# Optimization experiments

Hardware: AMD Instinct MI355X
Metric: run time of the kernel (lower is better)

Reference implementation:

```python
import jax, jax.numpy as jnp
import numpy as np

N_ADDR, N_TX = 150000, 200000
IN_DIM, HID, HEADS = 64, 32, 4
DIM = HID // HEADS
E_AT, E_TA, E_AA = 1000000, 1000000, 500000
SLOPE = 0.2  # HANConv default negative_slope


def setup_inputs() -> dict:
    key = jax.random.key(0)
    ks = jax.random.split(key, 16)
    f = lambda k, shape, s: jax.random.normal(k, shape, dtype=jnp.float32) * s
    return {
        "x_addr": f(ks[0], (N_ADDR, IN_DIM), 1.0),
        "x_tx": f(ks[1], (N_TX, IN_DIM), 1.0),
        "e_at_src": jax.random.randint(ks[2], (E_AT,), 0, N_ADDR, dtype=jnp.int32),
        "e_at_dst": jax.random.randint(ks[3], (E_AT,), 0, N_TX, dtype=jnp.int32),
        "e_ta_src": jax.random.randint(ks[4], (E_TA,), 0, N_TX, dtype=jnp.int32),
        "e_ta_dst": jax.random.randint(ks[5], (E_TA,), 0, N_ADDR, dtype=jnp.int32),
        "e_aa_src": jax.random.randint(ks[6], (E_AA,), 0, N_ADDR, dtype=jnp.int32),
        "e_aa_dst": jax.random.randint(ks[7], (E_AA,), 0, N_ADDR, dtype=jnp.int32),
        "pW1": f(ks[8], (2, IN_DIM, HID), 0.1),      # layer-1 proj per node type [addr, tx]
        "pb1": jnp.zeros((2, HID), jnp.float32),
        "pW23": f(ks[9], (2, 2, HID, HID), 0.1),     # [layer-1, node_type]
        "pb23": jnp.zeros((2, 2, HID), jnp.float32),
        "att_src": f(ks[10], (3, 3, HEADS, DIM), 0.1),  # [layer, edge_type, H, D]
        "att_dst": f(ks[11], (3, 3, HEADS, DIM), 0.1),
        "kW": f(ks[12], (3, HID, HID), 0.1),         # semantic k_lin per layer
        "kb": jnp.zeros((3, HID), jnp.float32),
        "q": f(ks[13], (3, HID), 0.1),               # semantic query per layer
        "linW": f(ks[14], (HID, 2), 0.1),
        "linb": jnp.zeros((2,), jnp.float32),
    }


def _edge_softmax(logits, dst, n):
    # numerically stable segment softmax over destination neighborhoods
    m = jax.ops.segment_max(logits, dst, num_segments=n)          # [n, H]
    m = jnp.where(jnp.isfinite(m), m, 0.0)
    e = jnp.exp(logits - m[dst])
    s = jax.ops.segment_sum(e, dst, num_segments=n)
    return e / (s[dst] + 1e-16)


def _relation(h_src, h_dst, src, dst, a_s, a_d, n_dst):
    alpha_src = jnp.einsum('nhd,hd->nh', h_src, a_s)
    alpha_dst = jnp.einsum('nhd,hd->nh', h_dst, a_d)
    logit = alpha_src[src] + alpha_dst[dst]                        # [E, H]
    logit = jnp.where(logit >= 0, logit, SLOPE * logit)            # leaky_relu
    alpha = _edge_softmax(logit, dst, n_dst)
    msg = h_src[src] * alpha[:, :, None]                           # [E, H, D]
    out = jax.ops.segment_sum(msg, dst, num_segments=n_dst)        # [n_dst, H, D]
    return jax.nn.relu(out.reshape(n_dst, HID))


def _semantic(xs, kW, kb, q):
    # xs: [R, N, F]; semantic-level attention over R relations (PyG `group`)
    t = jnp.tanh(xs @ kW + kb).mean(axis=1)       # [R, F]
    attn = jax.nn.softmax((t * q).sum(-1))        # [R]
    return jnp.einsum('r,rnf->nf', attn, xs)


def _han_layer(x_a, x_t, Wa, ba, Wt, bt, a_s, a_d, kW, kb, q, edges):
    h_a = (x_a @ Wa + ba).reshape(-1, HEADS, DIM)
    h_t = (x_t @ Wt + bt).reshape(-1, HEADS, DIM)
    o_tx = _relation(h_a, h_t, edges[0], edges[1], a_s[0], a_d[0], N_TX)
    o_a1 = _relation(h_t, h_a, edges[2], edges[3], a_s[1], a_d[1], N_ADDR)
    o_a2 = _relation(h_a, h_a, edges[4], edges[5], a_s[2], a_d[2], N_ADDR)
    new_a = _semantic(jnp.stack([o_a1, o_a2]), kW, kb, q)
    new_t = _semantic(o_tx[None], kW, kb, q)
    return new_a, new_t


def reference(x_addr, x_tx, e_at_src, e_at_dst, e_ta_src, e_ta_dst,
              e_aa_src, e_aa_dst, pW1, pb1, pW23, pb23, att_src, att_dst,
              kW, kb, q, linW, linb):
    edges = (e_at_src, e_at_dst, e_ta_src, e_ta_dst, e_aa_src, e_aa_dst)
    a, t = _han_layer(x_addr, x_tx, pW1[0], pb1[0], pW1[1], pb1[1],
                      att_src[0], att_dst[0], kW[0], kb[0], q[0], edges)
    a, t = jax.nn.relu(a), jax.nn.relu(t)  # wrapper relu; dropout = eval identity
    for l in range(2):
        a, t = _han_layer(a, t, pW23[l, 0], pb23[l, 0], pW23[l, 1], pb23[l, 1],
                          att_src[l + 1], att_dst[l + 1],
                          kW[l + 1], kb[l + 1], q[l + 1], edges)
        a, t = jax.nn.relu(a), jax.nn.relu(t)
    return a @ linW + linb
```

## Files before the change

### kernel.cpp

```cpp
#include <hip/hip_runtime.h>
#include <hip/hip_bf16.h>
#include <hip/hip_fp16.h>

#define NA 150000
#define NT 200000
#define E_AT 1000000
#define E_TA 1000000
#define E_AA 500000

#define CHK 4096
#define CAP 8192
#define P_AT 391
#define P_TA 293
#define P_AA 293
#define NBINS (P_AT + P_TA + P_AA)
#define CB_AT 245
#define CB_TA 245
#define CB_AA 123
#define NBBIN (CB_AT + CB_TA + CB_AA)

#define GB_AT 6250
#define GB_TA 4688
#define GB_AA 4688

#define GA32 4688
#define GT32 6250
#define NB_SEM 586

#define WO_W1   0
#define WO_B1   4096
#define WO_W23  4160
#define WO_B23  8256
#define WO_AS   8384
#define WO_AD   8672
#define WO_KW   8960
#define WO_KB   12032
#define WO_Q    12128
#define WO_LW   12224
#define WO_LB   12288

__device__ __forceinline__ float ldf(const void* p, long i, int f32) {
    if (f32) return ((const float*)p)[i];
    unsigned int u = ((const unsigned short*)p)[i];
    union { unsigned int ui; float f; } v; v.ui = u << 16;
    return v.f;
}
__device__ __forceinline__ float bf2f(unsigned short u) {
    union { unsigned int ui; float f; } v; v.ui = ((unsigned int)u) << 16;
    return v.f;
}
__device__ __forceinline__ float h2f(unsigned short u) {
    return __half2float(__ushort_as_half(u));
}
__device__ __forceinline__ unsigned short f2h(float x) {
    return __half_as_ushort(__float2half(x));
}
__device__ __forceinline__ float ftanh(float x) {
    x = fminf(fmaxf(x, -9.f), 9.f);
    float e = __expf(2.f * x);
    return (e - 1.f) / (e + 1.f);
}

__global__ void k_init(const void* __restrict__ x,
                       const void* __restrict__ pW1, const void* __restrict__ pb1,
                       const void* __restrict__ pW23, const void* __restrict__ pb23,
                       const void* __restrict__ attS, const void* __restrict__ attD,
                       const void* __restrict__ kW, const void* __restrict__ kb,
                       const void* __restrict__ qv, const void* __restrict__ linW,
                       const void* __restrict__ linb,
                       float* __restrict__ wts, int* __restrict__ flagp,
                       int* __restrict__ gcnt, float* __restrict__ sem) {
    __shared__ int cnt;
    const int t = threadIdx.x;
    if (t == 0) cnt = 0;
    __syncthreads();
    const unsigned short* u = (const unsigned short*)x;
    int wild = 0;
    for (int i = t; i < 4096; i += 256) {
        unsigned short v = u[i];
        int e = (v >> 7) & 0xFF;
        if (e > 133 || (e != 0 && e < 100)) wild++;
        else if (e == 0 && (v & 0x7F)) wild++;
    }
    atomicAdd(&cnt, wild);
    __syncthreads();
    const int f32 = (cnt > 1024) ? 1 : 0;
    if (t == 0) *flagp = f32;
    if (t < 8) sem[t] = 0.f;
    for (int i = t; i < 1024; i += 256) gcnt[i] = 0;
    for (int i = t; i < 4096; i += 256) wts[WO_W1 + i]  = ldf(pW1, i, f32);
    for (int i = t; i < 64;   i += 256) wts[WO_B1 + i]  = ldf(pb1, i, f32);
    for (int i = t; i < 4096; i += 256) wts[WO_W23 + i] = ldf(pW23, i, f32);
    for (int i = t; i < 128;  i += 256) wts[WO_B23 + i] = ldf(pb23, i, f32);
    for (int i = t; i < 288;  i += 256) wts[WO_AS + i]  = ldf(attS, i, f32);
    for (int i = t; i < 288;  i += 256) wts[WO_AD + i]  = ldf(attD, i, f32);
    for (int i = t; i < 3072; i += 256) wts[WO_KW + i]  = ldf(kW, i, f32);
    for (int i = t; i < 96;   i += 256) wts[WO_KB + i]  = ldf(kb, i, f32);
    for (int i = t; i < 96;   i += 256) wts[WO_Q + i]   = ldf(qv, i, f32);
    for (int i = t; i < 64;   i += 256) wts[WO_LW + i]  = ldf(linW, i, f32);
    for (int i = t; i < 2;    i += 256) wts[WO_LB + i]  = ldf(linb, i, f32);
}

__global__ __launch_bounds__(256) void k_projbin(
        const void* __restrict__ Xa, const void* __restrict__ Xt,
        const float* __restrict__ W, const float* __restrict__ Bv,
        unsigned short* __restrict__ Ha, unsigned short* __restrict__ Ht,
        const float* __restrict__ attD,
        float* __restrict__ ad0, float* __restrict__ ad1, float* __restrict__ ad2,
        const int* __restrict__ flagp,
        const int* __restrict__ eat_s, const int* __restrict__ eat_d,
        const int* __restrict__ eta_s, const int* __restrict__ eta_d,
        const int* __restrict__ eaa_s, const int* __restrict__ eaa_d,
        int* __restrict__ gcnt,
        int* __restrict__ slot_at, int* __restrict__ slot_ta, int* __restrict__ slot_aa) {
    __shared__ float smem[4224];
    const int t = threadIdx.x;
    int b = blockIdx.x;
    if (b < NBBIN) {
        int* hist = (int*)smem;
        const int *src, *dst; int E, P, seg; int* slot;
        if (b < CB_AT)              { src = eat_s; dst = eat_d; E = E_AT; P = P_AT; seg = 0;            slot = slot_at; }
        else if (b < CB_AT + CB_TA) { b -= CB_AT;  src = eta_s; dst = eta_d; E = E_TA; P = P_TA; seg = P_AT;        slot = slot_ta; }
        else                        { b -= CB_AT + CB_TA; src = eaa_s; dst = eaa_d; E = E_AA; P = P_AA; seg = P_AT + P_TA; slot = slot_aa; }
        long e0 = (long)b * CHK;
        for (int i = t; i < P; i += 256) hist[i] = 0;
        __syncthreads();
        for (int k = 0; k < CHK; k += 256) {
            long e = e0 + k + t;
            if (e < E) atomicAdd(&hist[dst[e] >> 9], 1);
        }
        __syncthreads();
        for (int i = t; i < P; i += 256) {
            int v = hist[i];
            hist[i] = atomicAdd(&gcnt[seg + i], v);
        }
        __syncthreads();
        for (int k = 0; k < CHK; k += 256) {
            long e = e0 + k + t;
            if (e < E) {
                int d = dst[e];
                int bin = d >> 9;
                int pos = atomicAdd(&hist[bin], 1);
                slot[bin * CAP + pos] = ((d & 511) << 18) | src[e];
            }
        }
        return;
    }
    b -= NBBIN;
    constexpr int K = 64, XS = K + 4, CPR = K / 4, TOT4 = 32 * CPR;
    float* Xs = smem;
    float* Wl = smem + 2176;
    const bool isA = b < GA32;
    const int bb = isA ? b : b - GA32;
    const int N = isA ? NA : NT;
    const int wOff = isA ? 0 : 2048;
    const int bOff = isA ? 0 : 32;
    const long n0 = (long)bb * 32;
    for (int i = t; i < K * 32; i += 256) Wl[i] = W[wOff + i];
    {
        const void* X = isA ? Xa : Xt;
        const int f32 = *flagp;
        if (f32) {
            const float* Xf = (const float*)X;
            for (int i = t; i < TOT4; i += 256) {
                int r = i / CPR, c = (i - r * CPR) * 4;
                long gr = n0 + r; if (gr >= N) gr = N - 1;
                *(float4*)&Xs[r * XS + c] = *(const float4*)&Xf[gr * K + c];
            }
        } else {
            const unsigned short* Xh = (const unsigned short*)X;
            for (int i = t; i < TOT4; i += 256) {
                int r = i / CPR, c = (i - r * CPR) * 4;
                long gr = n0 + r; if (gr >= N) gr = N - 1;
                ushort4 v = *(const ushort4*)&Xh[gr * K + c];
                float4 o;
                o.x = bf2f(v.x); o.y = bf2f(v.y); o.z = bf2f(v.z); o.w = bf2f(v.w);
                *(float4*)&Xs[r * XS + c] = o;
            }
        }
    }
    __syncthreads();
    const int g = t >> 3, q = t & 7;
    const long n = n0 + g;
    float a0 = Bv[bOff + q * 4 + 0];
    float a1 = Bv[bOff + q * 4 + 1];
    float a2 = Bv[bOff + q * 4 + 2];
    float a3 = Bv[bOff + q * 4 + 3];
#pragma unroll 4
    for (int k4 = 0; k4 < K; k4 += 4) {
        float4 xv = *(const float4*)&Xs[g * XS + k4];
        float4 w0 = *(const float4*)&Wl[(k4 + 0) * 32 + q * 4];
        float4 w1 = *(const float4*)&Wl[(k4 + 1) * 32 + q * 4];
        float4 w2 = *(const float4*)&Wl[(k4 + 2) * 32 + q * 4];
        float4 w3 = *(const float4*)&Wl[(k4 + 3) * 32 + q * 4];
        a0 = fmaf(xv.x, w0.x, a0); a1 = fmaf(xv.x, w0.y, a1);
        a2 = fmaf(xv.x, w0.z, a2); a3 = fmaf(xv.x, w0.w, a3);
        a0 = fmaf(xv.y, w1.x, a0); a1 = fmaf(xv.y, w1.y, a1);
        a2 = fmaf(xv.y, w1.z, a2); a3 = fmaf(xv.y, w1.w, a3);
        a0 = fmaf(xv.z, w2.x, a0); a1 = fmaf(xv.z, w2.y, a1);
        a2 = fmaf(xv.z, w2.z, a2); a3 = fmaf(xv.z, w2.w, a3);
        a0 = fmaf(xv.w, w3.x, a0); a1 = fmaf(xv.w, w3.y, a1);
        a2 = fmaf(xv.w, w3.z, a2); a3 = fmaf(xv.w, w3.w, a3);
    }
    if (n < N) {
        unsigned short* Hh = isA ? Ha : Ht;
        unsigned int p01 = (unsigned)f2h(a0) | ((unsigned)f2h(a1) << 16);
        unsigned int p23 = (unsigned)f2h(a2) | ((unsigned)f2h(a3) << 16);
        *(uint2*)&Hh[n * 32 + q * 4] = make_uint2(p01, p23);
        const int hh = q >> 1;
        const int ai = q * 4;
        if (isA) {
            float p1 = a0 * attD[ai + 32] + a1 * attD[ai + 33]
                     + a2 * attD[ai + 34] + a3 * attD[ai + 35];
            float p2 = a0 * attD[ai + 64] + a1 * attD[ai + 65]
                     + a2 * attD[ai + 66] + a3 * attD[ai + 67];
            float s1 = p1 + __shfl_xor(p1, 1);
            float s2 = p2 + __shfl_xor(p2, 1);
            if (!(q & 1)) { ad1[n * 4 + hh] = s1; ad2[n * 4 + hh] = s2; }
        } else {
            float p0 = a0 * attD[ai] + a1 * attD[ai + 1]
                     + a2 * attD[ai + 2] + a3 * attD[ai + 3];
            float s0 = p0 + __shfl_xor(p0, 1);
            if (!(q & 1)) ad0[n * 4 + hh] = s0;
        }
    }
}

__global__ __launch_bounds__(256) void k_proj2(
        const float* __restrict__ O1, const float* __restrict__ Ot,
        const float* __restrict__ O2, const float* __restrict__ semL,
        const float* __restrict__ W, int wOffA, int wOffT,
        const float* __restrict__ Bv, int bOffA, int bOffT,
        unsigned short* __restrict__ Ha, unsigned short* __restrict__ Ht,
        const float* __restrict__ attD, int lBase,
        float* __restrict__ ad0, float* __restrict__ ad1, float* __restrict__ ad2) {
    constexpr int K = 32, XS = K + 4, CPR = K / 4, TOT4 = 32 * CPR;
    __shared__ float Xs[32 * XS];
    __shared__ float Wl[K * 32];
    const int t = threadIdx.x;
    const bool isA = blockIdx.x < GA32;
    const int bb = isA ? (int)blockIdx.x : (int)blockIdx.x - GA32;
    const int N = isA ? NA : NT;
    const int wOff = isA ? wOffA : wOffT;
    const int bOff = isA ? bOffA : bOffT;
    const long n0 = (long)bb * 32;
    for (int i = t; i < K * 32; i += 256) Wl[i] = W[wOff + i];
    if (isA) {
        float s0 = semL[0] * (1.0f / NA), s1 = semL[1] * (1.0f / NA);
        float m = fmaxf(s0, s1);
        float e0 = __expf(s0 - m), e1 = __expf(s1 - m);
        float inv = 1.f / (e0 + e1);
        const float w0 = e0 * inv, w1 = e1 * inv;
        for (int i = t; i < TOT4; i += 256) {
            int r = i / CPR, c = (i - r * CPR) * 4;
            long gr = n0 + r; if (gr >= N) gr = N - 1;
            float4 va = *(const float4*)&O1[gr * K + c];
            float4 vb = *(const float4*)&O2[gr * K + c];
            float4 o;
            o.x = fmaxf(w0 * va.x + w1 * vb.x, 0.f);
            o.y = fmaxf(w0 * va.y + w1 * vb.y, 0.f);
            o.z = fmaxf(w0 * va.z + w1 * vb.z, 0.f);
            o.w = fmaxf(w0 * va.w + w1 * vb.w, 0.f);
            *(float4*)&Xs[r * XS + c] = o;
        }
    } else {
        for (int i = t; i < TOT4; i += 256) {
            int r = i / CPR, c = (i - r * CPR) * 4;
            long gr = n0 + r; if (gr >= N) gr = N - 1;
            *(float4*)&Xs[r * XS + c] = *(const float4*)&Ot[gr * K + c];
        }
    }
    __syncthreads();
    const int g = t >> 3, q = t & 7;
    const long n = n0 + g;
    float a0 = Bv[bOff + q * 4 + 0];
    float a1 = Bv[bOff + q * 4 + 1];
    float a2 = Bv[bOff + q * 4 + 2];
    float a3 = Bv[bOff + q * 4 + 3];
#pragma unroll 4
    for (int k4 = 0; k4 < K; k4 += 4) {
        float4 xv = *(const float4*)&Xs[g * XS + k4];
        float4 w0 = *(const float4*)&Wl[(k4 + 0) * 32 + q * 4];
        float4 w1 = *(const float4*)&Wl[(k4 + 1) * 32 + q * 4];
        float4 w2 = *(const float4*)&Wl[(k4 + 2) * 32 + q * 4];
        float4 w3 = *(const float4*)&Wl[(k4 + 3) * 32 + q * 4];
        a0 = fmaf(xv.x, w0.x, a0); a1 = fmaf(xv.x, w0.y, a1);
        a2 = fmaf(xv.x, w0.z, a2); a3 = fmaf(xv.x, w0.w, a3);
        a0 = fmaf(xv.y, w1.x, a0); a1 = fmaf(xv.y, w1.y, a1);
        a2 = fmaf(xv.y, w1.z, a2); a3 = fmaf(xv.y, w1.w, a3);
        a0 = fmaf(xv.z, w2.x, a0); a1 = fmaf(xv.z, w2.y, a1);
        a2 = fmaf(xv.z, w2.z, a2); a3 = fmaf(xv.z, w2.w, a3);
        a0 = fmaf(xv.w, w3.x, a0); a1 = fmaf(xv.w, w3.y, a1);
        a2 = fmaf(xv.w, w3.z, a2); a3 = fmaf(xv.w, w3.w, a3);
    }
    if (n < N) {
        unsigned short* Hh = isA ? Ha : Ht;
        unsigned int p01 = (unsigned)f2h(a0) | ((unsigned)f2h(a1) << 16);
        unsigned int p23 = (unsigned)f2h(a2) | ((unsigned)f2h(a3) << 16);
        *(uint2*)&Hh[n * 32 + q * 4] = make_uint2(p01, p23);
        const int hh = q >> 1;
        const int ai = lBase + q * 4;
        if (isA) {
            float p1 = a0 * attD[ai + 32] + a1 * attD[ai + 33]
                     + a2 * attD[ai + 34] + a3 * attD[ai + 35];
            float p2 = a0 * attD[ai + 64] + a1 * attD[ai + 65]
                     + a2 * attD[ai + 66] + a3 * attD[ai + 67];
            float s1 = p1 + __shfl_xor(p1, 1);
            float s2 = p2 + __shfl_xor(p2, 1);
            if (!(q & 1)) { ad1[n * 4 + hh] = s1; ad2[n * 4 + hh] = s2; }
        } else {
            float p0 = a0 * attD[ai] + a1 * attD[ai + 1]
                     + a2 * attD[ai + 2] + a3 * attD[ai + 3];
            float s0 = p0 + __shfl_xor(p0, 1);
            if (!(q & 1)) ad0[n * 4 + hh] = s0;
        }
    }
}

__global__ void k_binscan(const int* __restrict__ gcnt, int* __restrict__ bbase,
                          int* __restrict__ off_at, int* __restrict__ off_ta,
                          int* __restrict__ off_aa) {
    __shared__ int sa[512], sb[512];
    int t = threadIdx.x;
    const int segs[4] = {0, P_AT, P_AT + P_TA, NBINS};
    for (int r = 0; r < 3; r++) {
        int s0 = segs[r], P = segs[r + 1] - s0;
        sa[t] = (t < P) ? gcnt[s0 + t] : 0;
        __syncthreads();
        int* in = sa; int* out = sb;
        for (int o = 1; o < 512; o <<= 1) {
            out[t] = in[t] + (t >= o ? in[t - o] : 0);
            __syncthreads();
            int* tmp = in; in = out; out = tmp;
        }
        if (t < P) bbase[s0 + t] = (t ? in[t - 1] : 0);
        __syncthreads();
    }
    if (t == 0) { off_at[NT] = E_AT; off_ta[NA] = E_TA; off_aa[NA] = E_AA; }
}

__global__ __launch_bounds__(256) void k_binsort(
        const int* __restrict__ gcnt, const int* __restrict__ bbase,
        const int* __restrict__ slot_at, const int* __restrict__ slot_ta,
        const int* __restrict__ slot_aa,
        int* __restrict__ off_at, int* __restrict__ off_ta, int* __restrict__ off_aa,
        int* __restrict__ csr_at, int* __restrict__ csr_ta, int* __restrict__ csr_aa) {
    __shared__ int sa[512], sb[512], cur[512];
    int b = blockIdx.x, t = threadIdx.x;
    const int* slot; int* off; int* csr; int N, bin, seg;
    if (b < P_AT)              { slot = slot_at; off = off_at; csr = csr_at; N = NT; bin = b;                seg = 0; }
    else if (b < P_AT + P_TA)  { slot = slot_ta; off = off_ta; csr = csr_ta; N = NA; bin = b - P_AT;         seg = P_AT; }
    else                       { slot = slot_aa; off = off_aa; csr = csr_aa; N = NA; bin = b - P_AT - P_TA;  seg = P_AT + P_TA; }
    const int cnt  = gcnt[seg + bin];
    const int base = bbase[seg + bin];
    const int* sp = &slot[bin * CAP];
    sa[t] = 0; sa[t + 256] = 0;
    __syncthreads();
    for (int i = t; i < cnt; i += 256) atomicAdd(&sa[sp[i] >> 18], 1);
    __syncthreads();
    int* in = sa; int* out = sb;
    for (int o = 1; o < 512; o <<= 1) {
        for (int i = t; i < 512; i += 256)
            out[i] = in[i] + (i >= o ? in[i - o] : 0);
        __syncthreads();
        int* tmp = in; in = out; out = tmp;
    }
    for (int i = t; i < 512; i += 256) {
        int excl = i ? in[i - 1] : 0;
        cur[i] = excl;
        int gd = bin * 512 + i;
        if (gd < N) off[gd] = base + excl;
    }
    __syncthreads();
    for (int i = t; i < cnt; i += 256) {
        int pk = sp[i];
        int pos = atomicAdd(&cur[pk >> 18], 1);
        csr[base + pos] = pk & 0x3FFFF;
    }
}

__global__ __launch_bounds__(256) void k_gather3(
        const int* __restrict__ off_at, const int* __restrict__ csr_at,
        const int* __restrict__ off_ta, const int* __restrict__ csr_ta,
        const int* __restrict__ off_aa, const int* __restrict__ csr_aa,
        const float* __restrict__ ad0, const float* __restrict__ ad1,
        const float* __restrict__ ad2,
        const unsigned short* __restrict__ h_a, const unsigned short* __restrict__ h_t,
        float* __restrict__ o_tx, float* __restrict__ o_a1, float* __restrict__ o_a2,
        const float* __restrict__ attS, int lBase) {
    int b = blockIdx.x;
    const int *off, *csr;
    const float *ad_;
    const unsigned short* Hs;
    float* O;
    int N, attOff;
    if (b < GB_AT) {
        off = off_at; csr = csr_at; ad_ = ad0; Hs = h_a; O = o_tx; N = NT;
        attOff = lBase;
    } else if (b < GB_AT + GB_TA) {
        b -= GB_AT;
        off = off_ta; csr = csr_ta; ad_ = ad1; Hs = h_t; O = o_a1; N = NA;
        attOff = lBase + 32;
    } else {
        b -= GB_AT + GB_TA;
        off = off_aa; csr = csr_aa; ad_ = ad2; Hs = h_a; O = o_a2; N = NA;
        attOff = lBase + 64;
    }
    const int t = threadIdx.x;
    const int q = t & 7;
    const int hh = q >> 1;
    const int n = b * 32 + (t >> 3);
    if (n >= N) return;
    const float4 aq = *(const float4*)&attS[attOff + q * 4];
    const float aq0 = aq.x, aq1 = aq.y, aq2 = aq.z, aq3 = aq.w;
    const float adv = ad_[n * 4 + hh];
    const int p0 = off[n], p1 = off[n + 1];
    float ax = 0.f, ay = 0.f, az = 0.f, aw = 0.f, se = 0.f;
    int p = p0;
    for (; p + 4 <= p1; p += 4) {
        int s0 = csr[p], s1 = csr[p + 1], s2 = csr[p + 2], s3 = csr[p + 3];
        ushort4 v0 = *(const ushort4*)&Hs[s0 * 32 + q * 4];
        ushort4 v1 = *(const ushort4*)&Hs[s1 * 32 + q * 4];
        ushort4 v2 = *(const ushort4*)&Hs[s2 * 32 + q * 4];
        ushort4 v3 = *(const ushort4*)&Hs[s3 * 32 + q * 4];
        float h00 = h2f(v0.x), h01 = h2f(v0.y), h02 = h2f(v0.z), h03 = h2f(v0.w);
        float h10 = h2f(v1.x), h11 = h2f(v1.y), h12 = h2f(v1.z), h13 = h2f(v1.w);
        float h20 = h2f(v2.x), h21 = h2f(v2.y), h22 = h2f(v2.z), h23 = h2f(v2.w);
        float h30 = h2f(v3.x), h31 = h2f(v3.y), h32 = h2f(v3.z), h33 = h2f(v3.w);
        float pt0 = h00 * aq0 + h01 * aq1 + h02 * aq2 + h03 * aq3;
        float pt1 = h10 * aq0 + h11 * aq1 + h12 * aq2 + h13 * aq3;
        float pt2 = h20 * aq0 + h21 * aq1 + h22 * aq2 + h23 * aq3;
        float pt3 = h30 * aq0 + h31 * aq1 + h32 * aq2 + h33 * aq3;
        float al0 = pt0 + __shfl_xor(pt0, 1);
        float al1 = pt1 + __shfl_xor(pt1, 1);
        float al2 = pt2 + __shfl_xor(pt2, 1);
        float al3 = pt3 + __shfl_xor(pt3, 1);
        float l0 = al0 + adv; l0 = fmaxf(l0, 0.2f * l0); float e0 = __expf(l0);
        float l1 = al1 + adv; l1 = fmaxf(l1, 0.2f * l1); float e1 = __expf(l1);
        float l2 = al2 + adv; l2 = fmaxf(l2, 0.2f * l2); float e2 = __expf(l2);
        float l3 = al3 + adv; l3 = fmaxf(l3, 0.2f * l3); float e3 = __expf(l3);
        se += e0 + e1 + e2 + e3;
        ax += e0 * h00 + e1 * h10 + e2 * h20 + e3 * h30;
        ay += e0 * h01 + e1 * h11 + e2 * h21 + e3 * h31;
        az += e0 * h02 + e1 * h12 + e2 * h22 + e3 * h32;
        aw += e0 * h03 + e1 * h13 + e2 * h23 + e3 * h33;
    }
    for (; p < p1; p++) {
        int s = csr[p];
        ushort4 v = *(const ushort4*)&Hs[s * 32 + q * 4];
        float h0 = h2f(v.x), h1 = h2f(v.y), h2 = h2f(v.z), h3 = h2f(v.w);
        float pt = h0 * aq0 + h1 * aq1 + h2 * aq2 + h3 * aq3;
        float al = pt + __shfl_xor(pt, 1);
        float l = al + adv; l = fmaxf(l, 0.2f * l);
        float e = __expf(l);
        se += e;
        ax += e * h0; ay += e * h1; az += e * h2; aw += e * h3;
    }
    const float inv = 1.f / (se + 1e-16f);
    float4 r;
    r.x = fmaxf(ax * inv, 0.f);
    r.y = fmaxf(ay * inv, 0.f);
    r.z = fmaxf(az * inv, 0.f);
    r.w = fmaxf(aw * inv, 0.f);
    *(float4*)&O[n * 32 + q * 4] = r;
}

__global__ __launch_bounds__(256) void k_sem_reduce(
        const float* __restrict__ O1, const float* __restrict__ O2,
        const float* __restrict__ kWl, const float* __restrict__ kbl,
        const float* __restrict__ qvl, float* __restrict__ semL) {
    __shared__ float w[1088];
    __shared__ float bacc;
    const int t = threadIdx.x;
    const int r = (blockIdx.x >= NB_SEM) ? 1 : 0;
    const float* O = r ? O2 : O1;
    for (int i = t; i < 1024; i += 256) w[i] = kWl[i];
    if (t < 32) w[1024 + t] = kbl[t];
    if (t >= 64 && t < 96) w[1056 + (t - 64)] = qvl[t - 64];
    if (t == 0) bacc = 0.f;
    __syncthreads();
    long n = (long)(blockIdx.x - r * NB_SEM) * 256 + t;
    float S = 0.f;
    if (n < NA) {
        float x[32];
#pragma unroll
        for (int k = 0; k < 32; k++) x[k] = O[n * 32 + k];
#pragma unroll
        for (int f = 0; f < 32; f++) {
            float acc = w[1024 + f];
#pragma unroll
            for (int k = 0; k < 32; k++) acc += x[k] * w[k * 32 + f];
            S += ftanh(acc) * w[1056 + f];
        }
    }
    for (int o = 32; o > 0; o >>= 1) S += __shfl_xor(S, o, 64);
    if ((t & 63) == 0) atomicAdd(&bacc, S);
    __syncthreads();
    if (t == 0) atomicAdd(&semL[r], bacc);
}

__global__ void k_combine_final(const float* __restrict__ o1, const float* __restrict__ o2,
                                const float* __restrict__ semL,
                                const float* __restrict__ linW, const float* __restrict__ linb,
                                void* __restrict__ out, int N, const int* __restrict__ flagp) {
    int n = blockIdx.x * blockDim.x + threadIdx.x;
    if (n >= N) return;
    int f32 = *flagp;
    float q0 = semL[0] * (1.0f / NA), q1 = semL[1] * (1.0f / NA);
    float m = fmaxf(q0, q1);
    float e0 = __expf(q0 - m), e1 = __expf(q1 - m);
    float ai = 1.f / (e0 + e1);
    float w0 = e0 * ai, w1 = e1 * ai;
    float s0 = linb[0], s1 = linb[1];
    const float* p1 = &o1[(long)n * 32];
    const float* p2 = &o2[(long)n * 32];
#pragma unroll
    for (int f = 0; f < 32; f++) {
        float v = w0 * p1[f] + w1 * p2[f];
        v = (v > 0.f) ? v : 0.f;
        s0 += v * linW[f * 2];
        s1 += v * linW[f * 2 + 1];
    }
    if (f32) { ((float*)out)[n * 2] = s0; ((float*)out)[n * 2 + 1] = s1; }
    else {
        ((__hip_bfloat16*)out)[n * 2] = __float2bfloat16(s0);
        ((__hip_bfloat16*)out)[n * 2 + 1] = __float2bfloat16(s1);
    }
}

static inline int gblocks(long n) { return (int)((n + 255) / 256); }

extern "C" void kernel_launch(void* const* d_in, const int* in_sizes, int n_in,
                              void* d_out, int out_size, void* d_ws, size_t ws_size,
                              hipStream_t stream) {
    const void* x_addr = d_in[0];
    const void* x_tx   = d_in[1];
    const int* eat_s = (const int*)d_in[2];
    const int* eat_d = (const int*)d_in[3];
    const int* eta_s = (const int*)d_in[4];
    const int* eta_d = (const int*)d_in[5];
    const int* eaa_s = (const int*)d_in[6];
    const int* eaa_d = (const int*)d_in[7];
    const void* pW1  = d_in[8];
    const void* pb1  = d_in[9];
    const void* pW23 = d_in[10];
    const void* pb23 = d_in[11];
    const void* attS = d_in[12];
    const void* attD = d_in[13];
    const void* kW   = d_in[14];
    const void* kb   = d_in[15];
    const void* qv   = d_in[16];
    const void* linW = d_in[17];
    const void* linb = d_in[18];

    const size_t NA32 = (size_t)NA * 32, NT32 = (size_t)NT * 32;
    const size_t NA4 = (size_t)NA * 4, NT4 = (size_t)NT * 4;

    float* ws    = (float*)d_ws;
    float* h_aF  = ws;
    float* h_tF  = h_aF + NA32;
    float* o_a1  = h_tF + NT32;
    float* o_a2  = o_a1 + NA32;
    float* o_tx  = o_a2 + NA32;
    float* ad1   = o_tx + NT32;
    float* ad2   = ad1 + NA4;
    float* ad0   = ad2 + NA4;
    float* sem   = ad0 + NT4;
    int*   flagp = (int*)(sem + 8);
    int*   off_at = flagp + 16;
    int*   off_ta = off_at + (NT + 1);
    int*   off_aa = off_ta + (NA + 1);
    int*   csr_at = off_aa + (NA + 1);
    int*   csr_ta = csr_at + E_AT;
    int*   csr_aa = csr_ta + E_TA;
    int*   gcnt   = csr_aa + E_AA;
    int*   bbase  = gcnt + 1024;
    int*   slot_at = bbase + 1024;
    int*   slot_ta = slot_at + P_AT * CAP;
    int*   slot_aa = slot_ta + P_TA * CAP;
    float* wts    = (float*)(slot_aa + (size_t)P_AA * CAP);

    unsigned short* h_a = (unsigned short*)h_aF;
    unsigned short* h_t = (unsigned short*)h_tF;

    k_init<<<1, 256, 0, stream>>>(x_addr, pW1, pb1, pW23, pb23, attS, attD,
                                  kW, kb, qv, linW, linb, wts, flagp, gcnt, sem);

    k_projbin<<<NBBIN + GA32 + GT32, 256, 0, stream>>>(
        x_addr, x_tx, wts + WO_W1, wts + WO_B1, h_a, h_t, wts + WO_AD,
        ad0, ad1, ad2, flagp,
        eat_s, eat_d, eta_s, eta_d, eaa_s, eaa_d,
        gcnt, slot_at, slot_ta, slot_aa);
    k_binscan<<<1, 512, 0, stream>>>(gcnt, bbase, off_at, off_ta, off_aa);
    k_binsort<<<NBINS, 256, 0, stream>>>(gcnt, bbase, slot_at, slot_ta, slot_aa,
                                         off_at, off_ta, off_aa, csr_at, csr_ta, csr_aa);

    for (int l = 0; l < 3; l++) {
        if (l > 0) {
            int wi = (l - 1) * 2;
            k_proj2<<<GA32 + GT32, 256, 0, stream>>>(
                o_a1, o_tx, o_a2, sem + 2 * (l - 1),
                wts + WO_W23, (wi + 0) * 1024, (wi + 1) * 1024,
                wts + WO_B23, (wi + 0) * 32, (wi + 1) * 32,
                h_a, h_t, wts + WO_AD, l * 96, ad0, ad1, ad2);
        }
        k_gather3<<<GB_AT + GB_TA + GB_AA, 256, 0, stream>>>(
            off_at, csr_at, off_ta, csr_ta, off_aa, csr_aa,
            ad0, ad1, ad2, h_a, h_t, o_tx, o_a1, o_a2, wts + WO_AS, l * 96);
        k_sem_reduce<<<2 * NB_SEM, 256, 0, stream>>>(
            o_a1, o_a2, wts + WO_KW + l * 1024, wts + WO_KB + l * 32,
            wts + WO_Q + l * 32, sem + 2 * l);
        if (l == 2) {
            k_combine_final<<<gblocks(NA), 256, 0, stream>>>(o_a1, o_a2, sem + 4,
                                                             wts + WO_LW, wts + WO_LB,
                                                             d_out, NA, flagp);
        }
    }
}
```

Baseline: 570.9 us.

## Fuse bin scan into binsort, gather two nodes per lane group, skip dead tx relation

Removes the single-block bin-scan kernel; each binsort block now computes its own base by summing the preceding bin counts with a block reduction. The gather kernel now has each 8-lane group handle two destination nodes, interleaving their edge loops so more independent loads are in flight, which halves the block count. In the last layer the tx-destination relation is skipped because its output is never used for the final address-node result. The costs are redundant prefix reads in binsort, more register pressure, and extra loop code paths in the gather.

```diff
diff --git a/kernel.cpp b/kernel.cpp
--- a/kernel.cpp
+++ b/kernel.cpp
@@ -19,9 +19,9 @@
 #define CB_AA 123
 #define NBBIN (CB_AT + CB_TA + CB_AA)
 
-#define GB_AT 6250
-#define GB_TA 4688
-#define GB_AA 4688
+#define GB2_AT 3125
+#define GB2_TA 2344
+#define GB2_AA 2344
 
 #define GA32 4688
 #define GT32 6250
@@ -317,45 +317,29 @@
     }
 }
 
-__global__ void k_binscan(const int* __restrict__ gcnt, int* __restrict__ bbase,
-                          int* __restrict__ off_at, int* __restrict__ off_ta,
-                          int* __restrict__ off_aa) {
-    __shared__ int sa[512], sb[512];
-    int t = threadIdx.x;
-    const int segs[4] = {0, P_AT, P_AT + P_TA, NBINS};
-    for (int r = 0; r < 3; r++) {
-        int s0 = segs[r], P = segs[r + 1] - s0;
-        sa[t] = (t < P) ? gcnt[s0 + t] : 0;
-        __syncthreads();
-        int* in = sa; int* out = sb;
-        for (int o = 1; o < 512; o <<= 1) {
-            out[t] = in[t] + (t >= o ? in[t - o] : 0);
-            __syncthreads();
-            int* tmp = in; in = out; out = tmp;
-        }
-        if (t < P) bbase[s0 + t] = (t ? in[t - 1] : 0);
-        __syncthreads();
-    }
-    if (t == 0) { off_at[NT] = E_AT; off_ta[NA] = E_TA; off_aa[NA] = E_AA; }
-}
-
 __global__ __launch_bounds__(256) void k_binsort(
-        const int* __restrict__ gcnt, const int* __restrict__ bbase,
+        const int* __restrict__ gcnt,
         const int* __restrict__ slot_at, const int* __restrict__ slot_ta,
         const int* __restrict__ slot_aa,
         int* __restrict__ off_at, int* __restrict__ off_ta, int* __restrict__ off_aa,
         int* __restrict__ csr_at, int* __restrict__ csr_ta, int* __restrict__ csr_aa) {
     __shared__ int sa[512], sb[512], cur[512];
+    __shared__ int red[4];
     int b = blockIdx.x, t = threadIdx.x;
     const int* slot; int* off; int* csr; int N, bin, seg;
     if (b < P_AT)              { slot = slot_at; off = off_at; csr = csr_at; N = NT; bin = b;                seg = 0; }
     else if (b < P_AT + P_TA)  { slot = slot_ta; off = off_ta; csr = csr_ta; N = NA; bin = b - P_AT;         seg = P_AT; }
     else                       { slot = slot_aa; off = off_aa; csr = csr_aa; N = NA; bin = b - P_AT - P_TA;  seg = P_AT + P_TA; }
+    if (b == 0 && t == 0) { off_at[NT] = E_AT; off_ta[NA] = E_TA; off_aa[NA] = E_AA; }
+    int part = 0;
+    for (int i = t; i < bin; i += 256) part += gcnt[seg + i];
+    for (int o = 32; o > 0; o >>= 1) part += __shfl_xor(part, o, 64);
+    if ((t & 63) == 0) red[t >> 6] = part;
+    sa[t] = 0; sa[t + 256] = 0;
+    __syncthreads();
+    const int base = red[0] + red[1] + red[2] + red[3];
     const int cnt  = gcnt[seg + bin];
-    const int base = bbase[seg + bin];
     const int* sp = &slot[bin * CAP];
-    sa[t] = 0; sa[t + 256] = 0;
-    __syncthreads();
     for (int i = t; i < cnt; i += 256) atomicAdd(&sa[sp[i] >> 18], 1);
     __syncthreads();
     int* in = sa; int* out = sb;
@@ -378,6 +362,43 @@
         csr[base + pos] = pk & 0x3FFFF;
     }
 }
+
+#define LD4(P, V0, V1, V2, V3) \
+    int s0_##V0 = csr[P], s1_##V0 = csr[(P) + 1], s2_##V0 = csr[(P) + 2], s3_##V0 = csr[(P) + 3]; \
+    ushort4 V0 = *(const ushort4*)&Hs[s0_##V0 * 32 + q * 4]; \
+    ushort4 V1 = *(const ushort4*)&Hs[s1_##V0 * 32 + q * 4]; \
+    ushort4 V2 = *(const ushort4*)&Hs[s2_##V0 * 32 + q * 4]; \
+    ushort4 V3 = *(const ushort4*)&Hs[s3_##V0 * 32 + q * 4];
+
+#define PR4(V0, V1, V2, V3, ADV, SE, AX, AY, AZ, AW) { \
+    float h00 = h2f(V0.x), h01 = h2f(V0.y), h02 = h2f(V0.z), h03 = h2f(V0.w); \
+    float h10 = h2f(V1.x), h11 = h2f(V1.y), h12 = h2f(V1.z), h13 = h2f(V1.w); \
+    float h20 = h2f(V2.x), h21 = h2f(V2.y), h22 = h2f(V2.z), h23 = h2f(V2.w); \
+    float h30 = h2f(V3.x), h31 = h2f(V3.y), h32 = h2f(V3.z), h33 = h2f(V3.w); \
+    float pt0 = h00 * aq0 + h01 * aq1 + h02 * aq2 + h03 * aq3; \
+    float pt1 = h10 * aq0 + h11 * aq1 + h12 * aq2 + h13 * aq3; \
+    float pt2 = h20 * aq0 + h21 * aq1 + h22 * aq2 + h23 * aq3; \
+    float pt3 = h30 * aq0 + h31 * aq1 + h32 * aq2 + h33 * aq3; \
+    float al0 = pt0 + __shfl_xor(pt0, 1); \
+    float al1 = pt1 + __shfl_xor(pt1, 1); \
+    float al2 = pt2 + __shfl_xor(pt2, 1); \
+    float al3 = pt3 + __shfl_xor(pt3, 1); \
+    float l0 = al0 + (ADV); l0 = fmaxf(l0, 0.2f * l0); float e0 = __expf(l0); \
+    float l1 = al1 + (ADV); l1 = fmaxf(l1, 0.2f * l1); float e1 = __expf(l1); \
+    float l2 = al2 + (ADV); l2 = fmaxf(l2, 0.2f * l2); float e2 = __expf(l2); \
+    float l3 = al3 + (ADV); l3 = fmaxf(l3, 0.2f * l3); float e3 = __expf(l3); \
+    SE += e0 + e1 + e2 + e3; \
+    AX += e0 * h00 + e1 * h10 + e2 * h20 + e3 * h30; \
+    AY += e0 * h01 + e1 * h11 + e2 * h21 + e3 * h31; \
+    AZ += e0 * h02 + e1 * h12 + e2 * h22 + e3 * h32; \
+    AW += e0 * h03 + e1 * h13 + e2 * h23 + e3 * h33; }
+
+#define PR1(V, ADV, SE, AX, AY, AZ, AW) { \
+    float h0 = h2f(V.x), h1 = h2f(V.y), h2v = h2f(V.z), h3 = h2f(V.w); \
+    float pt = h0 * aq0 + h1 * aq1 + h2v * aq2 + h3 * aq3; \
+    float al = pt + __shfl_xor(pt, 1); \
+    float l = al + (ADV); l = fmaxf(l, 0.2f * l); float e = __expf(l); \
+    SE += e; AX += e * h0; AY += e * h1; AZ += e * h2v; AW += e * h3; }
 
 __global__ __launch_bounds__(256) void k_gather3(
         const int* __restrict__ off_at, const int* __restrict__ csr_at,
@@ -387,82 +408,90 @@
         const float* __restrict__ ad2,
         const unsigned short* __restrict__ h_a, const unsigned short* __restrict__ h_t,
         float* __restrict__ o_tx, float* __restrict__ o_a1, float* __restrict__ o_a2,
-        const float* __restrict__ attS, int lBase) {
+        const float* __restrict__ attS, int lBase, int gbAT) {
     int b = blockIdx.x;
     const int *off, *csr;
     const float *ad_;
     const unsigned short* Hs;
     float* O;
     int N, attOff;
-    if (b < GB_AT) {
+    if (b < gbAT) {
         off = off_at; csr = csr_at; ad_ = ad0; Hs = h_a; O = o_tx; N = NT;
         attOff = lBase;
-    } else if (b < GB_AT + GB_TA) {
-        b -= GB_AT;
+    } else if (b < gbAT + GB2_TA) {
+        b -= gbAT;
         off = off_ta; csr = csr_ta; ad_ = ad1; Hs = h_t; O = o_a1; N = NA;
         attOff = lBase + 32;
     } else {
-        b -= GB_AT + GB_TA;
+        b -= gbAT + GB2_TA;
         off = off_aa; csr = csr_aa; ad_ = ad2; Hs = h_a; O = o_a2; N = NA;
         attOff = lBase + 64;
     }
     const int t = threadIdx.x;
     const int q = t & 7;
     const int hh = q >> 1;
-    const int n = b * 32 + (t >> 3);
-    if (n >= N) return;
-    const float4 aq = *(const float4*)&attS[attOff + q * 4];
-    const float aq0 = aq.x, aq1 = aq.y, aq2 = aq.z, aq3 = aq.w;
-    const float adv = ad_[n * 4 + hh];
-    const int p0 = off[n], p1 = off[n + 1];
-    float ax = 0.f, ay = 0.f, az = 0.f, aw = 0.f, se = 0.f;
-    int p = p0;
-    for (; p + 4 <= p1; p += 4) {
-        int s0 = csr[p], s1 = csr[p + 1], s2 = csr[p + 2], s3 = csr[p + 3];
-        ushort4 v0 = *(const ushort4*)&Hs[s0 * 32 + q * 4];
-        ushort4 v1 = *(const ushort4*)&Hs[s1 * 32 + q * 4];
-        ushort4 v2 = *(const ushort4*)&Hs[s2 * 32 + q * 4];
-        ushort4 v3 = *(const ushort4*)&Hs[s3 * 32 + q * 4];
-        float h00 = h2f(v0.x), h01 = h2f(v0.y), h02 = h2f(v0.z), h03 = h2f(v0.w);
-        float h10 = h2f(v1.x), h11 = h2f(v1.y), h12 = h2f(v1.z), h13 = h2f(v1.w);
-        float h20 = h2f(v2.x), h21 = h2f(v2.y), h22 = h2f(v2.z), h23 = h2f(v2.w);
-        float h30 = h2f(v3.x), h31 = h2f(v3.y), h32 = h2f(v3.z), h33 = h2f(v3.w);
-        float pt0 = h00 * aq0 + h01 * aq1 + h02 * aq2 + h03 * aq3;
-        float pt1 = h10 * aq0 + h11 * aq1 + h12 * aq2 + h13 * aq3;
-        float pt2 = h20 * aq0 + h21 * aq1 + h22 * aq2 + h23 * aq3;
-        float pt3 = h30 * aq0 + h31 * aq1 + h32 * aq2 + h33 * aq3;
-        float al0 = pt0 + __shfl_xor(pt0, 1);
-        float al1 = pt1 + __shfl_xor(pt1, 1);
-        float al2 = pt2 + __shfl_xor(pt2, 1);
-        float al3 = pt3 + __shfl_xor(pt3, 1);
-        float l0 = al0 + adv; l0 = fmaxf(l0, 0.2f * l0); float e0 = __expf(l0);
-        float l1 = al1 + adv; l1 = fmaxf(l1, 0.2f * l1); float e1 = __expf(l1);
-        float l2 = al2 + adv; l2 = fmaxf(l2, 0.2f * l2); float e2 = __expf(l2);
-        float l3 = al3 + adv; l3 = fmaxf(l3, 0.2f * l3); float e3 = __expf(l3);
-        se += e0 + e1 + e2 + e3;
-        ax += e0 * h00 + e1 * h10 + e2 * h20 + e3 * h30;
-        ay += e0 * h01 + e1 * h11 + e2 * h21 + e3 * h31;
-        az += e0 * h02 + e1 * h12 + e2 * h22 + e3 * h32;
-        aw += e0 * h03 + e1 * h13 + e2 * h23 + e3 * h33;
-    }
-    for (; p < p1; p++) {
-        int s = csr[p];
-        ushort4 v = *(const ushort4*)&Hs[s * 32 + q * 4];
-        float h0 = h2f(v.x), h1 = h2f(v.y), h2 = h2f(v.z), h3 = h2f(v.w);
-        float pt = h0 * aq0 + h1 * aq1 + h2 * aq2 + h3 * aq3;
-        float al = pt + __shfl_xor(pt, 1);
-        float l = al + adv; l = fmaxf(l, 0.2f * l);
-        float e = __expf(l);
-        se += e;
-        ax += e * h0; ay += e * h1; az += e * h2; aw += e * h3;
-    }
-    const float inv = 1.f / (se + 1e-16f);
-    float4 r;
-    r.x = fmaxf(ax * inv, 0.f);
-    r.y = fmaxf(ay * inv, 0.f);
-    r.z = fmaxf(az * inv, 0.f);
-    r.w = fmaxf(aw * inv, 0.f);
-    *(float4*)&O[n * 32 + q * 4] = r;
+    const int g = t >> 3;
+    const int n1 = b * 64 + g;
+    const int n2 = n1 + 32;
+    const float4 aqv = *(const float4*)&attS[attOff + q * 4];
+    const float aq0 = aqv.x, aq1 = aqv.y, aq2 = aqv.z, aq3 = aqv.w;
+    float adv1 = 0.f, adv2 = 0.f;
+    int pa = 0, ea = 0, pb = 0, eb = 0;
+    if (n1 < N) { adv1 = ad_[n1 * 4 + hh]; pa = off[n1]; ea = off[n1 + 1]; }
+    if (n2 < N) { adv2 = ad_[n2 * 4 + hh]; pb = off[n2]; eb = off[n2 + 1]; }
+    float ax1 = 0.f, ay1 = 0.f, az1 = 0.f, aw1 = 0.f, se1 = 0.f;
+    float ax2 = 0.f, ay2 = 0.f, az2 = 0.f, aw2 = 0.f, se2 = 0.f;
+    while (pa + 4 <= ea && pb + 4 <= eb) {
+        LD4(pa, va0, va1, va2, va3)
+        LD4(pb, vb0, vb1, vb2, vb3)
+        PR4(va0, va1, va2, va3, adv1, se1, ax1, ay1, az1, aw1)
+        PR4(vb0, vb1, vb2, vb3, adv2, se2, ax2, ay2, az2, aw2)
+        pa += 4; pb += 4;
+    }
+    for (; pa + 4 <= ea; pa += 4) {
+        LD4(pa, va0, va1, va2, va3)
+        PR4(va0, va1, va2, va3, adv1, se1, ax1, ay1, az1, aw1)
+    }
+    for (; pb + 4 <= eb; pb += 4) {
+        LD4(pb, vb0, vb1, vb2, vb3)
+        PR4(vb0, vb1, vb2, vb3, adv2, se2, ax2, ay2, az2, aw2)
+    }
+    while (pa < ea && pb < eb) {
+        int sA = csr[pa], sB = csr[pb];
+        ushort4 vA = *(const ushort4*)&Hs[sA * 32 + q * 4];
+        ushort4 vB = *(const ushort4*)&Hs[sB * 32 + q * 4];
+        PR1(vA, adv1, se1, ax1, ay1, az1, aw1)
+        PR1(vB, adv2, se2, ax2, ay2, az2, aw2)
+        pa++; pb++;
+    }
+    for (; pa < ea; pa++) {
+        int sA = csr[pa];
+        ushort4 vA = *(const ushort4*)&Hs[sA * 32 + q * 4];
+        PR1(vA, adv1, se1, ax1, ay1, az1, aw1)
+    }
+    for (; pb < eb; pb++) {
+        int sB = csr[pb];
+        ushort4 vB = *(const ushort4*)&Hs[sB * 32 + q * 4];
+        PR1(vB, adv2, se2, ax2, ay2, az2, aw2)
+    }
+    if (n1 < N) {
+        float inv = 1.f / (se1 + 1e-16f);
+        float4 r;
+        r.x = fmaxf(ax1 * inv, 0.f);
+        r.y = fmaxf(ay1 * inv, 0.f);
+        r.z = fmaxf(az1 * inv, 0.f);
+        r.w = fmaxf(aw1 * inv, 0.f);
+        *(float4*)&O[n1 * 32 + q * 4] = r;
+    }
+    if (n2 < N) {
+        float inv = 1.f / (se2 + 1e-16f);
+        float4 r;
+        r.x = fmaxf(ax2 * inv, 0.f);
+        r.y = fmaxf(ay2 * inv, 0.f);
+        r.z = fmaxf(az2 * inv, 0.f);
+        r.w = fmaxf(aw2 * inv, 0.f);
+        *(float4*)&O[n2 * 32 + q * 4] = r;
+    }
 }
 
 __global__ __launch_bounds__(256) void k_sem_reduce(
@@ -574,8 +603,7 @@
     int*   csr_ta = csr_at + E_AT;
     int*   csr_aa = csr_ta + E_TA;
     int*   gcnt   = csr_aa + E_AA;
-    int*   bbase  = gcnt + 1024;
-    int*   slot_at = bbase + 1024;
+    int*   slot_at = gcnt + 1024;
     int*   slot_ta = slot_at + P_AT * CAP;
     int*   slot_aa = slot_ta + P_TA * CAP;
     float* wts    = (float*)(slot_aa + (size_t)P_AA * CAP);
@@ -591,8 +619,7 @@
         ad0, ad1, ad2, flagp,
         eat_s, eat_d, eta_s, eta_d, eaa_s, eaa_d,
         gcnt, slot_at, slot_ta, slot_aa);
-    k_binscan<<<1, 512, 0, stream>>>(gcnt, bbase, off_at, off_ta, off_aa);
-    k_binsort<<<NBINS, 256, 0, stream>>>(gcnt, bbase, slot_at, slot_ta, slot_aa,
+    k_binsort<<<NBINS, 256, 0, stream>>>(gcnt, slot_at, slot_ta, slot_aa,
                                          off_at, off_ta, off_aa, csr_at, csr_ta, csr_aa);
 
     for (int l = 0; l < 3; l++) {
@@ -604,9 +631,10 @@
                 wts + WO_B23, (wi + 0) * 32, (wi + 1) * 32,
                 h_a, h_t, wts + WO_AD, l * 96, ad0, ad1, ad2);
         }
-        k_gather3<<<GB_AT + GB_TA + GB_AA, 256, 0, stream>>>(
+        const int gbAT = (l < 2) ? GB2_AT : 0;
+        k_gather3<<<gbAT + GB2_TA + GB2_AA, 256, 0, stream>>>(
             off_at, csr_at, off_ta, csr_ta, off_aa, csr_aa,
-            ad0, ad1, ad2, h_a, h_t, o_tx, o_a1, o_a2, wts + WO_AS, l * 96);
+            ad0, ad1, ad2, h_a, h_t, o_tx, o_a1, o_a2, wts + WO_AS, l * 96, gbAT);
         k_sem_reduce<<<2 * NB_SEM, 256, 0, stream>>>(
             o_a1, o_a2, wts + WO_KW + l * 1024, wts + WO_KB + l * 32,
             wts + WO_Q + l * 32, sem + 2 * l);
```

Result: slower. 591.1 us (+3.5%).
